# Optimization experiments

Hardware: AMD Instinct MI355X
Metric: run time of the kernel (lower is better)

## Reference

```python
import jax, jax.numpy as jnp
import numpy as np

N, IN_DIM, HID = 8192, 256, 512
NEG_INF = jnp.float32(-1e30)


def _linear_params(key, fan_in, fan_out):
    k1, k2 = jax.random.split(key)
    bound = 1.0 / np.sqrt(fan_in)
    W = jax.random.uniform(k1, (fan_in, fan_out), jnp.float32, -bound, bound)
    b = jax.random.uniform(k2, (fan_out,), jnp.float32, -bound, bound)
    return W, b


def setup_inputs() -> dict:
    key = jax.random.key(0)
    ks = jax.random.split(key, 10)
    x = jax.random.normal(ks[0], (N, IN_DIM), jnp.float32)
    adj = jax.random.randint(ks[1], (N, N), 0, 2) > 0
    adj = adj | jnp.eye(N, dtype=bool)  # self-loops: no all-masked rows
    Win, b_in = _linear_params(ks[2], IN_DIM, HID)
    Wq, bq = _linear_params(ks[3], HID, HID)
    Wk, bk = _linear_params(ks[4], HID, HID)
    Wv, bv = _linear_params(ks[5], HID, HID)
    Wo, bo = _linear_params(ks[6], HID, HID)
    Ws, bs = _linear_params(ks[7], HID, 1)
    Wf1, bf1 = _linear_params(ks[8], HID, HID)
    Wf2, bf2 = _linear_params(ks[9], HID, HID)
    g1 = jnp.ones((HID,), jnp.float32); be1 = jnp.zeros((HID,), jnp.float32)
    g2 = jnp.ones((HID,), jnp.float32); be2 = jnp.zeros((HID,), jnp.float32)
    return dict(x=x, adj=adj, Win=Win, b_in=b_in, Wq=Wq, bq=bq, Wk=Wk, bk=bk,
                Wv=Wv, bv=bv, Wo=Wo, bo=bo, Ws=Ws, bs=bs,
                g1=g1, be1=be1, g2=g2, be2=be2,
                Wf1=Wf1, bf1=bf1, Wf2=Wf2, bf2=bf2)


def _layernorm(x, g, b, eps=1e-5):
    mu = jnp.mean(x, axis=-1, keepdims=True)
    var = jnp.mean(jnp.square(x - mu), axis=-1, keepdims=True)
    return (x - mu) * jax.lax.rsqrt(var + eps) * g + b


def reference(x, adj, Win, b_in, Wq, bq, Wk, bk, Wv, bv, Wo, bo, Ws, bs,
              g1, be1, g2, be2, Wf1, bf1, Wf2, bf2):
    h = x @ Win + b_in                      # [N, HID]
    q = h @ Wq + bq
    k = h @ Wk + bk
    v = h @ Wv + bv
    scale = 1.0 / np.sqrt(HID).astype(np.float32)
    scores = (q @ k.T) * scale              # [N, N]
    scores = jnp.where(adj, scores, NEG_INF)
    attn = jax.nn.softmax(scores, axis=-1)  # dropout = identity (eval mode)
    h2 = attn @ v                           # [N, HID]
    h = _layernorm(h + (h2 @ Wo + bo), g1, be1)
    ff = jnp.maximum(h @ Wf1 + bf1, 0.0) @ Wf2 + bf2
    h = _layernorm(h + ff, g2, be2)
    logits = (h @ Ws + bs).squeeze(-1)      # [N]
    return logits
```

## Files before the change

kernel.cpp:

```cpp
#include <hip/hip_runtime.h>

typedef unsigned int u32;
typedef unsigned short u16;
typedef unsigned char u8;

typedef __bf16 bf16_t;
typedef bf16_t bf16x8 __attribute__((ext_vector_type(8)));
typedef float f32x4 __attribute__((ext_vector_type(4)));

#define NROW 8192
#define HID 512
#define DIN 256
#define LDQ 1536
#define NSPLIT 4
#define KVCH (NROW / NSPLIT)
#define KVB 64

__device__ __forceinline__ u16 f2b(float f) {
    u32 u = __float_as_uint(f);
    u32 r = (u + 0x7fffu + ((u >> 16) & 1u)) >> 16;
    return (u16)r;
}
__device__ __forceinline__ float b2f(u16 h) {
    return __uint_as_float(((u32)h) << 16);
}
__device__ __forceinline__ f32x4 zero4() {
    f32x4 z = {0.f, 0.f, 0.f, 0.f};
    return z;
}
__device__ __forceinline__ void gll16(const void* g, void* l) {
    __builtin_amdgcn_global_load_lds(
        (const __attribute__((address_space(1))) unsigned int*)g,
        (__attribute__((address_space(3))) unsigned int*)l, 16, 0, 0);
}

__global__ void sniff_adj(const u32* __restrict__ adj, int* __restrict__ mode) {
    __shared__ int f01[4], ff32[4], fbf[4];
    int t = threadIdx.x, lane = t & 63, wv = t >> 6;
    int all01 = 1, allf32 = 1, allbf = 1;
    for (int i = t; i < 1024; i += 256) {
        u32 w = adj[i];
        if (w > 1u) all01 = 0;
        if (w != 0u && w != 0x3f800000u) allf32 = 0;
    }
    const u16* h = (const u16*)adj;
    for (int i = t; i < 2048; i += 256) {
        u16 v = h[i];
        if (v != 0 && v != 0x3f80u) allbf = 0;
    }
    all01 = __all(all01);
    allf32 = __all(allf32);
    allbf = __all(allbf);
    if (lane == 0) { f01[wv] = all01; ff32[wv] = allf32; fbf[wv] = allbf; }
    __syncthreads();
    if (t == 0) {
        int a = f01[0] & f01[1] & f01[2] & f01[3];
        int b = ff32[0] & ff32[1] & ff32[2] & ff32[3];
        int c = fbf[0] & fbf[1] & fbf[2] & fbf[3];
        mode[0] = a ? 0 : (b ? 1 : (c ? 2 : 3));
    }
}

__global__ __launch_bounds__(256) void build_bits(const void* __restrict__ adj,
                                                  const int* __restrict__ mode,
                                                  u32* __restrict__ bits) {
    int row = blockIdx.x;
    int t = threadIdx.x;
    int lane = t & 63, wv = t >> 6;
    int md = *mode;
    for (int c0 = 0; c0 < NROW; c0 += 256) {
        int c = c0 + t;
        size_t idx = (size_t)row * NROW + c;
        bool nz;
        if (md == 0)      nz = ((const u32*)adj)[idx] != 0u;
        else if (md == 1) nz = ((const float*)adj)[idx] != 0.f;
        else if (md == 2) nz = ((const u16*)adj)[idx] != 0;
        else              nz = ((const u8*)adj)[idx] != 0;
        unsigned long long bm = __ballot(nz);
        if (lane == 0) {
            int w = row * 256 + (c0 >> 5) + wv * 2;
            bits[w] = (u32)bm;
            bits[w + 1] = (u32)(bm >> 32);
        }
    }
}

__global__ __launch_bounds__(256) void convert_f32_bf16(const float* __restrict__ in,
                                                        u16* __restrict__ out, int n) {
    int i = blockIdx.x * 256 + threadIdx.x;
    if (i < n) out[i] = f2b(in[i]);
}

__global__ __launch_bounds__(256) void transpose_wt(const float* __restrict__ W,
                                                    u16* __restrict__ out, int R, int C) {
    __shared__ u16 tile[64][65];
    int c0 = blockIdx.x * 64, r0 = blockIdx.y * 64;
    int t = threadIdx.x;
#pragma unroll
    for (int i = 0; i < 16; i++) {
        int idx = t + i * 256;
        int rr = idx >> 6, cc = idx & 63;
        tile[rr][cc] = f2b(W[(size_t)(r0 + rr) * C + c0 + cc]);
    }
    __syncthreads();
#pragma unroll
    for (int i = 0; i < 16; i++) {
        int idx = t + i * 256;
        int rr = idx >> 6, cc = idx & 63;
        out[(size_t)(c0 + rr) * R + r0 + cc] = tile[cc][rr];
    }
}

__global__ void concat_bias(const float* __restrict__ bq, const float* __restrict__ bk,
                            const float* __restrict__ bv, float* __restrict__ out) {
    int i = blockIdx.x * 256 + threadIdx.x;
    if (i >= 1536) return;
    out[i] = i < 512 ? bq[i] : (i < 1024 ? bk[i - 512] : bv[i - 1024]);
}

__global__ __launch_bounds__(256) void transpose_v_tiled(const u16* __restrict__ in, int ldv,
                                                         u16* __restrict__ out) {
    __shared__ u16 tl[64][72];
    int c0 = blockIdx.x * 64;
    int r0 = blockIdx.y * 64;
    int t = threadIdx.x;
#pragma unroll
    for (int i = 0; i < 2; i++) {
        int idx = t + i * 256;
        int rr = idx >> 3, ck = idx & 7;
        bf16x8 v = *(const bf16x8*)(in + (size_t)(r0 + rr) * ldv + c0 + ck * 8);
#pragma unroll
        for (int j = 0; j < 8; j++) tl[ck * 8 + j][rr] = ((u16*)&v)[j];
    }
    __syncthreads();
#pragma unroll
    for (int i = 0; i < 2; i++) {
        int idx = t + i * 256;
        int col = idx >> 3, ch = idx & 7;
        int kv = ch * 8;
        bf16x8 v;
#pragma unroll
        for (int j = 0; j < 8; j++) ((u16*)&v)[j] = tl[col][kv + j];
        *(bf16x8*)(out + (size_t)((r0 + kv) >> 5) * (HID * 32) +
                   (size_t)(c0 + col) * 32 + (kv & 31)) = v;
    }
}

__global__ __launch_bounds__(256, 3) void gemm_k(const u16* __restrict__ A, int lda,
                                                 const u16* __restrict__ Bt,
                                                 const float* __restrict__ bias,
                                                 const float* __restrict__ resid,
                                                 float* __restrict__ outF,
                                                 u16* __restrict__ outH, int ldo,
                                                 int relu, int K) {
    __shared__ u16 Ald[2][8192];
    __shared__ u16 Bld[2][4096];
    int t = threadIdx.x;
    int lane = t & 63, wave = t >> 6;
    int l15 = lane & 15, lg = lane >> 4;
    int row0 = blockIdx.y * 128, col0 = blockIdx.x * 64;

    auto stage = [&](int buf, int kk) {
#pragma unroll
        for (int p = 0; p < 4; p++) {
            int idx = p * 256 + t;
            int row = idx >> 3, c = idx & 7;
            gll16(A + (size_t)(row0 + row) * lda + kk + ((c ^ (row & 7)) * 8),
                  &Ald[buf][idx * 8]);
        }
#pragma unroll
        for (int p = 0; p < 2; p++) {
            int idx = p * 256 + t;
            int row = idx >> 3, c = idx & 7;
            gll16(Bt + (size_t)(col0 + row) * K + kk + ((c ^ (row & 7)) * 8),
                  &Bld[buf][idx * 8]);
        }
    };

    f32x4 acc[2][4];
#pragma unroll
    for (int i = 0; i < 2; i++)
#pragma unroll
        for (int j = 0; j < 4; j++) acc[i][j] = zero4();

    stage(0, 0);
    asm volatile("s_waitcnt vmcnt(0)" ::: "memory");
    __syncthreads();

    int nk = K >> 6;
    for (int kt = 0; kt < nk; kt++) {
        int buf = kt & 1;
        if (kt + 1 < nk) stage(buf ^ 1, (kt + 1) * 64);
#pragma unroll
        for (int ks = 0; ks < 2; ks++) {
            bf16x8 af[2], bfr[4];
#pragma unroll
            for (int i = 0; i < 2; i++) {
                int row = wave * 32 + i * 16 + l15;
                af[i] = *(const bf16x8*)&Ald[buf][row * 64 + (((ks * 4 + lg) ^ (row & 7)) * 8)];
            }
#pragma unroll
            for (int j = 0; j < 4; j++) {
                int row = j * 16 + l15;
                bfr[j] = *(const bf16x8*)&Bld[buf][row * 64 + (((ks * 4 + lg) ^ (row & 7)) * 8)];
            }
            __builtin_amdgcn_s_setprio(1);
#pragma unroll
            for (int i = 0; i < 2; i++)
#pragma unroll
                for (int j = 0; j < 4; j++)
                    acc[i][j] = __builtin_amdgcn_mfma_f32_16x16x32_bf16(af[i], bfr[j],
                                                                       acc[i][j], 0, 0, 0);
            __builtin_amdgcn_s_setprio(0);
        }
        asm volatile("s_waitcnt vmcnt(0)" ::: "memory");
        __syncthreads();
    }
#pragma unroll
    for (int j = 0; j < 4; j++) {
        int col = col0 + j * 16 + l15;
        float bv = bias[col];
#pragma unroll
        for (int i = 0; i < 2; i++) {
#pragma unroll
            for (int r = 0; r < 4; r++) {
                int row = row0 + wave * 32 + i * 16 + lg * 4 + r;
                float v = acc[i][j][r] + bv;
                if (relu) v = fmaxf(v, 0.f);
                size_t o = (size_t)row * ldo + col;
                if (resid) v += resid[o];
                if (outF) outF[o] = v;
                if (outH) outH[o] = f2b(v);
            }
        }
    }
}

__global__ __launch_bounds__(512, 2) void attn_kernel(const u16* __restrict__ QKV,
                                                      const u16* __restrict__ VTt,
                                                      const u32* __restrict__ bits,
                                                      u16* __restrict__ Opart,
                                                      float* __restrict__ Mpart,
                                                      float* __restrict__ Lpart) {
    extern __shared__ char smem[];
    u16* Klds = (u16*)smem;
    u16* Plds = (u16*)(smem + 131072);
    float* cscL = (float*)(smem + 147456);
    int* flagsL = (int*)(smem + 147968);
    int lane = threadIdx.x & 63, wave = threadIdx.x >> 6;
    int l15 = lane & 15, lg = lane >> 4;
    int s = blockIdx.x & 3;
    int qb = blockIdx.x >> 2;
    int qrow0 = qb * 128;
    int myrows = qrow0 + wave * 16;
    const u16* Kg = QKV + 512;

    bf16x8 qf[16];
    {
        const u16* qp = QKV + (size_t)(myrows + l15) * LDQ + lg * 8;
#pragma unroll
        for (int ks = 0; ks < 16; ks++) qf[ks] = *(const bf16x8*)(qp + ks * 32);
    }

    f32x4 acc[8][4];
#pragma unroll
    for (int i = 0; i < 8; i++)
#pragma unroll
        for (int j = 0; j < 4; j++) acc[i][j] = zero4();
    float m[4] = {-1e30f, -1e30f, -1e30f, -1e30f};
    float lsum[4] = {0.f, 0.f, 0.f, 0.f};
    const float scale = 0.04419417382415922f;
    int kvbeg = s * KVCH;

    auto STAGE = [&](int buf, int kv0) {
#pragma unroll
        for (int i = 0; i < 8; i++) {
            int seg = wave * 8 + i;
            int ks = seg >> 2, q = seg & 3;
            gll16(Kg + (size_t)(kv0 + q * 16 + l15) * LDQ + ks * 32 + lg * 8,
                  Klds + buf * 32768 + seg * 512 + lane * 8);
        }
    };

    STAGE(0, kvbeg);
    asm volatile("s_waitcnt vmcnt(0)" ::: "memory");
    __syncthreads();

    const int NT = KVCH / KVB;
    for (int t = 0; t < NT; ++t) {
        int kv0 = kvbeg + t * KVB;
        int buf = t & 1;
        const u16* kb = Klds + buf * 32768;

        f32x4 sf[4];
#pragma unroll
        for (int f = 0; f < 4; f++) sf[f] = zero4();
        __builtin_amdgcn_s_setprio(1);
#pragma unroll
        for (int ks = 0; ks < 16; ks++) {
#pragma unroll
            for (int q = 0; q < 4; q++) {
                bf16x8 b = *(const bf16x8*)(kb + (ks * 4 + q) * 512 + lane * 8);
                sf[q] = __builtin_amdgcn_mfma_f32_16x16x32_bf16(qf[ks], b, sf[q], 0, 0, 0);
            }
        }
        __builtin_amdgcn_s_setprio(0);

        u32 w0[4], w1[4];
#pragma unroll
        for (int r = 0; r < 4; r++) {
            const u32* wp = bits + (size_t)(myrows + lg * 4 + r) * 256 + (kv0 >> 5);
            w0[r] = wp[0];
            w1[r] = wp[1];
        }
        float pvv[4][4];
        float mx[4] = {-1e30f, -1e30f, -1e30f, -1e30f};
#pragma unroll
        for (int f = 0; f < 4; f++) {
            int c = f * 16 + l15;
#pragma unroll
            for (int r = 0; r < 4; r++) {
                u32 w = (c < 32) ? w0[r] : w1[r];
                bool bit = (w >> (c & 31)) & 1u;
                float sv = bit ? sf[f][r] * scale : -1e30f;
                pvv[f][r] = sv;
                mx[r] = fmaxf(mx[r], sv);
            }
        }
        bool need = false;
#pragma unroll
        for (int r = 0; r < 4; r++) need |= (mx[r] > m[r] + 8.0f);
        int wneed = __any(need ? 1 : 0);
        float cscv[4] = {1.f, 1.f, 1.f, 1.f};
        if (wneed) {
#pragma unroll
            for (int r = 0; r < 4; r++) {
#pragma unroll
                for (int off = 8; off; off >>= 1)
                    mx[r] = fmaxf(mx[r], __shfl_xor(mx[r], off, 64));
                float mn = fmaxf(m[r], mx[r]);
                cscv[r] = __expf(m[r] - mn);
                m[r] = mn;
                lsum[r] *= cscv[r];
            }
        }
        if (l15 == 0) *(f32x4*)&cscL[wave * 16 + lg * 4] = *(f32x4*)cscv;
        if (lane == 0) flagsL[wave] = wneed;

#pragma unroll
        for (int f = 0; f < 4; f++)
#pragma unroll
            for (int r = 0; r < 4; r++)
                pvv[f][r] = (pvv[f][r] < -1e29f) ? 0.f : __expf(pvv[f][r] - m[r]);
#pragma unroll
        for (int r = 0; r < 4; r++)
            lsum[r] += pvv[0][r] + pvv[1][r] + pvv[2][r] + pvv[3][r];

#pragma unroll
        for (int f = 0; f < 4; f++)
#pragma unroll
            for (int r = 0; r < 4; r++)
                Plds[(wave * 2 + (f >> 1)) * 512 + ((f & 1) * 2 + (l15 >> 3)) * 128 +
                     (lg * 4 + r) * 8 + (l15 & 7)] = f2b(pvv[f][r]);

        asm volatile("s_waitcnt lgkmcnt(0)" ::: "memory");
        __builtin_amdgcn_sched_barrier(0);
        __builtin_amdgcn_s_barrier();
        __builtin_amdgcn_sched_barrier(0);

        if (t + 1 < NT) STAGE(buf ^ 1, kv0 + KVB);

        int anyf = __any(flagsL[lane & 7] != 0);
        if (anyf) {
#pragma unroll
            for (int rf = 0; rf < 8; rf++) {
                f32x4 cs = *(const f32x4*)&cscL[rf * 16 + lg * 4];
#pragma unroll
                for (int cf = 0; cf < 4; cf++) {
                    f32x4 a = acc[rf][cf];
                    a[0] *= cs[0]; a[1] *= cs[1]; a[2] *= cs[2]; a[3] *= cs[3];
                    acc[rf][cf] = a;
                }
            }
        }

#pragma unroll
        for (int ks = 0; ks < 2; ks++) {
            const u16* vbase = VTt + (size_t)((kv0 >> 5) + ks) * (HID * 32) +
                               (size_t)wave * 64 * 32;
            bf16x8 vv[4];
#pragma unroll
            for (int cf = 0; cf < 4; cf++)
                vv[cf] = *(const bf16x8*)(vbase + (size_t)(cf * 16 + l15) * 32 + lg * 8);
            __builtin_amdgcn_s_setprio(1);
#pragma unroll
            for (int rf = 0; rf < 8; rf++) {
                bf16x8 pa = *(const bf16x8*)(Plds + (rf * 2 + ks) * 512 + lane * 8);
#pragma unroll
                for (int cf = 0; cf < 4; cf++)
                    acc[rf][cf] = __builtin_amdgcn_mfma_f32_16x16x32_bf16(pa, vv[cf],
                                                                         acc[rf][cf], 0, 0, 0);
            }
            __builtin_amdgcn_s_setprio(0);
        }

        asm volatile("s_waitcnt vmcnt(0) lgkmcnt(0)" ::: "memory");
        __builtin_amdgcn_sched_barrier(0);
        __builtin_amdgcn_s_barrier();
        __builtin_amdgcn_sched_barrier(0);
    }

#pragma unroll
    for (int r = 0; r < 4; r++) {
#pragma unroll
        for (int off = 8; off; off >>= 1)
            lsum[r] += __shfl_xor(lsum[r], off, 64);
    }
    if (l15 == 0) {
#pragma unroll
        for (int r = 0; r < 4; r++) {
            size_t o = (size_t)s * NROW + myrows + lg * 4 + r;
            Mpart[o] = m[r];
            Lpart[o] = lsum[r];
        }
    }
#pragma unroll
    for (int rf = 0; rf < 8; rf++)
#pragma unroll
        for (int cf = 0; cf < 4; cf++) {
            int col = wave * 64 + cf * 16 + l15;
#pragma unroll
            for (int j = 0; j < 4; j++) {
                size_t row = (size_t)s * NROW + qrow0 + rf * 16 + lg * 4 + j;
                Opart[row * HID + col] = f2b(acc[rf][cf][j]);
            }
        }
}

__global__ __launch_bounds__(256) void attn_combine(const u16* __restrict__ Opart,
                                                    const float* __restrict__ Mpart,
                                                    const float* __restrict__ Lpart,
                                                    u16* __restrict__ O16) {
    int idx = blockIdx.x * 256 + threadIdx.x;
    int row = idx >> 6;
    int c8 = (idx & 63) << 3;
    float ms[NSPLIT], M = -1e30f;
#pragma unroll
    for (int s = 0; s < NSPLIT; s++) {
        ms[s] = Mpart[(size_t)s * NROW + row];
        M = fmaxf(M, ms[s]);
    }
    float w[NSPLIT], L = 0.f;
#pragma unroll
    for (int s = 0; s < NSPLIT; s++) {
        w[s] = __expf(ms[s] - M);
        L += Lpart[(size_t)s * NROW + row] * w[s];
    }
    float inv = 1.f / L;
    float o[8];
#pragma unroll
    for (int j = 0; j < 8; j++) o[j] = 0.f;
#pragma unroll
    for (int s = 0; s < NSPLIT; s++) {
        bf16x8 p = *(const bf16x8*)(Opart + ((size_t)s * NROW + row) * HID + c8);
#pragma unroll
        for (int j = 0; j < 8; j++) o[j] += (float)p[j] * w[s];
    }
    bf16x8 res;
#pragma unroll
    for (int j = 0; j < 8; j++) {
        u16 b = f2b(o[j] * inv);
        res[j] = *(bf16_t*)&b;
    }
    *(bf16x8*)(O16 + (size_t)row * HID + c8) = res;
}

__global__ __launch_bounds__(256) void ln_single(const float* __restrict__ a,
                                                 const float* __restrict__ g,
                                                 const float* __restrict__ be,
                                                 float* __restrict__ outF,
                                                 u16* __restrict__ outH) {
    int row = blockIdx.x, t = threadIdx.x;
    const float* ar = a + (size_t)row * HID;
    float x0 = ar[t];
    float x1 = ar[t + 256];
    float s = x0 + x1, s2 = x0 * x0 + x1 * x1;
#pragma unroll
    for (int off = 32; off; off >>= 1) {
        s += __shfl_xor(s, off, 64);
        s2 += __shfl_xor(s2, off, 64);
    }
    __shared__ float ls[4], ls2[4];
    int wv = t >> 6, ln = t & 63;
    if (ln == 0) { ls[wv] = s; ls2[wv] = s2; }
    __syncthreads();
    float S = ls[0] + ls[1] + ls[2] + ls[3];
    float S2 = ls2[0] + ls2[1] + ls2[2] + ls2[3];
    float mu = S * (1.f / 512.f);
    float var = S2 * (1.f / 512.f) - mu * mu;
    float inv = rsqrtf(var + 1e-5f);
    float y0 = (x0 - mu) * inv * g[t] + be[t];
    float y1 = (x1 - mu) * inv * g[t + 256] + be[t + 256];
    size_t o = (size_t)row * HID + t;
    if (outF) { outF[o] = y0; outF[o + 256] = y1; }
    if (outH) { outH[o] = f2b(y0); outH[o + 256] = f2b(y1); }
}

__global__ __launch_bounds__(256) void logits_k(const u16* __restrict__ hfin,
                                                const float* __restrict__ Ws,
                                                const float* __restrict__ bs,
                                                float* __restrict__ out) {
    int row = blockIdx.x * 4 + (threadIdx.x >> 6);
    int lane = threadIdx.x & 63;
    const u16* hp = hfin + (size_t)row * HID + lane * 8;
    float sum = 0.f;
#pragma unroll
    for (int j = 0; j < 8; j++) sum += b2f(hp[j]) * Ws[lane * 8 + j];
#pragma unroll
    for (int off = 32; off; off >>= 1) sum += __shfl_xor(sum, off, 64);
    if (lane == 0) out[row] = sum + bs[0];
}

extern "C" void kernel_launch(void* const* d_in, const int* in_sizes, int n_in,
                              void* d_out, int out_size, void* d_ws, size_t ws_size,
                              hipStream_t stream) {
    const float* x   = (const float*)d_in[0];
    const void*  adj = d_in[1];
    const float* Win = (const float*)d_in[2];
    const float* b_in= (const float*)d_in[3];
    const float* Wq  = (const float*)d_in[4];
    const float* bq  = (const float*)d_in[5];
    const float* Wk  = (const float*)d_in[6];
    const float* bk  = (const float*)d_in[7];
    const float* Wv  = (const float*)d_in[8];
    const float* bv  = (const float*)d_in[9];
    const float* Wo  = (const float*)d_in[10];
    const float* bo  = (const float*)d_in[11];
    const float* Ws  = (const float*)d_in[12];
    const float* bs  = (const float*)d_in[13];
    const float* g1  = (const float*)d_in[14];
    const float* be1 = (const float*)d_in[15];
    const float* g2  = (const float*)d_in[16];
    const float* be2 = (const float*)d_in[17];
    const float* Wf1 = (const float*)d_in[18];
    const float* bf1 = (const float*)d_in[19];
    const float* Wf2 = (const float*)d_in[20];
    const float* bf2 = (const float*)d_in[21];

    char* ws = (char*)d_ws;
    const size_t MB = 1u << 20;
    const size_t OFF_PART = 0;
    const size_t OFF_X16  = 0;
    const size_t OFF_H16  = 4 * MB;
    const size_t OFF_HN32 = 12 * MB;
    const size_t OFF_HN16 = 28 * MB;
    const size_t OFF_FF1  = 4 * MB;
    const size_t OFF_HF32 = 36 * MB;
    const size_t OFF_QKV  = 52 * MB;
    const size_t OFF_OP32 = 52 * MB;
    const size_t OFF_FF2  = 52 * MB;
    const size_t OFF_VT   = 76 * MB;
    const size_t OFF_HFIN = 76 * MB;
    const size_t OFF_H2   = 84 * MB;
    const size_t OFF_BITS = 92 * MB;
    size_t off = 100 * MB;
    const size_t OFF_WINT = off;  off += 262144;
    const size_t OFF_QKVT = off;  off += 1572864;
    const size_t OFF_WOT  = off;  off += 524288;
    const size_t OFF_WF1T = off;  off += 524288;
    const size_t OFF_WF2T = off;  off += 524288;
    const size_t OFF_BQKV = off;  off += 8192;
    const size_t OFF_MODE = off;  off += 4096;
    const size_t OFF_MPART= off;  off += 131072;
    const size_t OFF_LPART= off;  off += 131072;

    u16* pX16   = (u16*)(ws + OFF_X16);
    u16* pH16   = (u16*)(ws + OFF_H16);
    float* pHN32= (float*)(ws + OFF_HN32);
    u16* pHN16  = (u16*)(ws + OFF_HN16);
    u16* pFF1   = (u16*)(ws + OFF_FF1);
    float* pHF32= (float*)(ws + OFF_HF32);
    u16* pQKV   = (u16*)(ws + OFF_QKV);
    float* pOP32= (float*)(ws + OFF_OP32);
    float* pFF2 = (float*)(ws + OFF_FF2);
    u16* pVT    = (u16*)(ws + OFF_VT);
    u16* pHFIN  = (u16*)(ws + OFF_HFIN);
    u16* pH2    = (u16*)(ws + OFF_H2);
    u32* pBits  = (u32*)(ws + OFF_BITS);
    u16* pPart  = (u16*)(ws + OFF_PART);
    u16* pWinT  = (u16*)(ws + OFF_WINT);
    u16* pQKVT  = (u16*)(ws + OFF_QKVT);
    u16* pWoT   = (u16*)(ws + OFF_WOT);
    u16* pWf1T  = (u16*)(ws + OFF_WF1T);
    u16* pWf2T  = (u16*)(ws + OFF_WF2T);
    float* pBqkv= (float*)(ws + OFF_BQKV);
    int* pMode  = (int*)(ws + OFF_MODE);
    float* pMp  = (float*)(ws + OFF_MPART);
    float* pLp  = (float*)(ws + OFF_LPART);

    sniff_adj<<<1, 256, 0, stream>>>((const u32*)adj, pMode);
    build_bits<<<NROW, 256, 0, stream>>>(adj, pMode, pBits);

    convert_f32_bf16<<<(NROW * DIN) / 256, 256, 0, stream>>>(x, pX16, NROW * DIN);
    transpose_wt<<<dim3(8, 4), 256, 0, stream>>>(Win, pWinT, DIN, HID);
    transpose_wt<<<dim3(8, 8), 256, 0, stream>>>(Wq, pQKVT, HID, HID);
    transpose_wt<<<dim3(8, 8), 256, 0, stream>>>(Wk, pQKVT + 512 * 512, HID, HID);
    transpose_wt<<<dim3(8, 8), 256, 0, stream>>>(Wv, pQKVT + 2 * 512 * 512, HID, HID);
    transpose_wt<<<dim3(8, 8), 256, 0, stream>>>(Wo, pWoT, HID, HID);
    transpose_wt<<<dim3(8, 8), 256, 0, stream>>>(Wf1, pWf1T, HID, HID);
    transpose_wt<<<dim3(8, 8), 256, 0, stream>>>(Wf2, pWf2T, HID, HID);
    concat_bias<<<6, 256, 0, stream>>>(bq, bk, bv, pBqkv);

    gemm_k<<<dim3(8, 64), 256, 0, stream>>>(pX16, DIN, pWinT, b_in, nullptr,
                                            pHF32, pH16, HID, 0, DIN);
    gemm_k<<<dim3(24, 64), 256, 0, stream>>>(pH16, HID, pQKVT, pBqkv, nullptr,
                                             nullptr, pQKV, LDQ, 0, HID);
    transpose_v_tiled<<<dim3(HID / 64, NROW / 64), 256, 0, stream>>>(pQKV + 1024, LDQ, pVT);
    attn_kernel<<<64 * NSPLIT, 512, 148032, stream>>>(pQKV, pVT, pBits, pPart, pMp, pLp);
    attn_combine<<<NROW * HID / (256 * 8), 256, 0, stream>>>(pPart, pMp, pLp, pH2);
    gemm_k<<<dim3(8, 64), 256, 0, stream>>>(pH2, HID, pWoT, bo, pHF32,
                                            pOP32, nullptr, HID, 0, HID);
    ln_single<<<NROW, 256, 0, stream>>>(pOP32, g1, be1, pHN32, pHN16);
    gemm_k<<<dim3(8, 64), 256, 0, stream>>>(pHN16, HID, pWf1T, bf1, nullptr,
                                            nullptr, pFF1, HID, 1, HID);
    gemm_k<<<dim3(8, 64), 256, 0, stream>>>(pFF1, HID, pWf2T, bf2, pHN32,
                                            pFF2, nullptr, HID, 0, HID);
    ln_single<<<NROW, 256, 0, stream>>>(pFF2, g2, be2, nullptr, pHFIN);
    logits_k<<<NROW / 4, 256, 0, stream>>>(pHFIN, Ws, bs, (float*)d_out);
}
```

Baseline: 502.1 us.

## Retile attention to 64-row, 4-wave blocks and fuse prep and final LN kernels

The attention kernel now runs 4-wave blocks on 64 query rows with 32-key tiles, so LDS use per block roughly halves and twice as many blocks launch. Each wave now owns 128 output columns instead of 64. Separately, the weight transposes, x conversion and bias concat are merged into one prep launch, and the second layernorm is fused with the logits dot product. Together these cut launch overhead and an intermediate bf16 buffer. The smaller tiles mean more loop iterations and barriers per key, and the V fragment loads are reused across fewer query rows.

```diff
diff --git a/kernel.cpp b/kernel.cpp
--- a/kernel.cpp
+++ b/kernel.cpp
@@ -14,7 +14,7 @@
 #define LDQ 1536
 #define NSPLIT 4
 #define KVCH (NROW / NSPLIT)
-#define KVB 64
+#define KVB 32
 
 __device__ __forceinline__ u16 f2b(float f) {
     u32 u = __float_as_uint(f);
@@ -34,9 +34,13 @@
         (__attribute__((address_space(3))) unsigned int*)l, 16, 0, 0);
 }
 
-__global__ void sniff_adj(const u32* __restrict__ adj, int* __restrict__ mode) {
+__global__ void sniff_and_bias(const u32* __restrict__ adj, int* __restrict__ mode,
+                               const float* __restrict__ bq, const float* __restrict__ bk,
+                               const float* __restrict__ bv, float* __restrict__ bqkv) {
     __shared__ int f01[4], ff32[4], fbf[4];
     int t = threadIdx.x, lane = t & 63, wv = t >> 6;
+    for (int i = t; i < 1536; i += 256)
+        bqkv[i] = i < 512 ? bq[i] : (i < 1024 ? bk[i - 512] : bv[i - 1024]);
     int all01 = 1, allf32 = 1, allbf = 1;
     for (int i = t; i < 1024; i += 256) {
         u32 w = adj[i];
@@ -85,37 +89,59 @@
     }
 }
 
-__global__ __launch_bounds__(256) void convert_f32_bf16(const float* __restrict__ in,
-                                                        u16* __restrict__ out, int n) {
-    int i = blockIdx.x * 256 + threadIdx.x;
-    if (i < n) out[i] = f2b(in[i]);
-}
-
-__global__ __launch_bounds__(256) void transpose_wt(const float* __restrict__ W,
-                                                    u16* __restrict__ out, int R, int C) {
+__global__ __launch_bounds__(256) void prep(const float* __restrict__ x,
+                                            const float* __restrict__ Win,
+                                            const float* __restrict__ Wq,
+                                            const float* __restrict__ Wk,
+                                            const float* __restrict__ Wv,
+                                            const float* __restrict__ Wo,
+                                            const float* __restrict__ Wf1,
+                                            const float* __restrict__ Wf2,
+                                            u16* __restrict__ pX16,
+                                            u16* __restrict__ pWinT,
+                                            u16* __restrict__ pQKVT,
+                                            u16* __restrict__ pWoT,
+                                            u16* __restrict__ pWf1T,
+                                            u16* __restrict__ pWf2T) {
+    int z = blockIdx.z;
+    int t = threadIdx.x;
+    if (z == 7) {
+        size_t base = ((size_t)blockIdx.y * 8 + blockIdx.x) * 32768;
+#pragma unroll 4
+        for (int k = 0; k < 128; k++) {
+            size_t i = base + k * 256 + t;
+            pX16[i] = f2b(x[i]);
+        }
+        return;
+    }
+    const float* src;
+    u16* dst;
+    int R = 512;
+    switch (z) {
+        case 0: src = Win; dst = pWinT; R = 256; break;
+        case 1: src = Wq;  dst = pQKVT; break;
+        case 2: src = Wk;  dst = pQKVT + 512 * 512; break;
+        case 3: src = Wv;  dst = pQKVT + 2 * 512 * 512; break;
+        case 4: src = Wo;  dst = pWoT; break;
+        case 5: src = Wf1; dst = pWf1T; break;
+        default: src = Wf2; dst = pWf2T; break;
+    }
+    int r0 = blockIdx.y * 64, c0 = blockIdx.x * 64;
+    if (r0 >= R) return;
     __shared__ u16 tile[64][65];
-    int c0 = blockIdx.x * 64, r0 = blockIdx.y * 64;
-    int t = threadIdx.x;
 #pragma unroll
     for (int i = 0; i < 16; i++) {
         int idx = t + i * 256;
         int rr = idx >> 6, cc = idx & 63;
-        tile[rr][cc] = f2b(W[(size_t)(r0 + rr) * C + c0 + cc]);
+        tile[rr][cc] = f2b(src[(size_t)(r0 + rr) * 512 + c0 + cc]);
     }
     __syncthreads();
 #pragma unroll
     for (int i = 0; i < 16; i++) {
         int idx = t + i * 256;
         int rr = idx >> 6, cc = idx & 63;
-        out[(size_t)(c0 + rr) * R + r0 + cc] = tile[cc][rr];
-    }
-}
-
-__global__ void concat_bias(const float* __restrict__ bq, const float* __restrict__ bk,
-                            const float* __restrict__ bv, float* __restrict__ out) {
-    int i = blockIdx.x * 256 + threadIdx.x;
-    if (i >= 1536) return;
-    out[i] = i < 512 ? bq[i] : (i < 1024 ? bk[i - 512] : bv[i - 1024]);
+        dst[(size_t)(c0 + rr) * R + r0 + cc] = tile[cc][rr];
+    }
 }
 
 __global__ __launch_bounds__(256) void transpose_v_tiled(const u16* __restrict__ in, int ldv,
@@ -236,7 +262,7 @@
     }
 }
 
-__global__ __launch_bounds__(512, 2) void attn_kernel(const u16* __restrict__ QKV,
+__global__ __launch_bounds__(256, 2) void attn_kernel(const u16* __restrict__ QKV,
                                                       const u16* __restrict__ VTt,
                                                       const u32* __restrict__ bits,
                                                       u16* __restrict__ Opart,
@@ -244,14 +270,14 @@
                                                       float* __restrict__ Lpart) {
     extern __shared__ char smem[];
     u16* Klds = (u16*)smem;
-    u16* Plds = (u16*)(smem + 131072);
-    float* cscL = (float*)(smem + 147456);
-    int* flagsL = (int*)(smem + 147968);
+    u16* Plds = (u16*)(smem + 65536);
+    float* cscL = (float*)(smem + 69632);
+    int* flagsL = (int*)(smem + 69888);
     int lane = threadIdx.x & 63, wave = threadIdx.x >> 6;
     int l15 = lane & 15, lg = lane >> 4;
-    int s = blockIdx.x & 3;
-    int qb = blockIdx.x >> 2;
-    int qrow0 = qb * 128;
+    int s = blockIdx.x >> 7;
+    int qb = blockIdx.x & 127;
+    int qrow0 = qb * 64;
     int myrows = qrow0 + wave * 16;
     const u16* Kg = QKV + 512;
 
@@ -262,11 +288,11 @@
         for (int ks = 0; ks < 16; ks++) qf[ks] = *(const bf16x8*)(qp + ks * 32);
     }
 
-    f32x4 acc[8][4];
-#pragma unroll
-    for (int i = 0; i < 8; i++)
-#pragma unroll
-        for (int j = 0; j < 4; j++) acc[i][j] = zero4();
+    f32x4 acc[4][8];
+#pragma unroll
+    for (int i = 0; i < 4; i++)
+#pragma unroll
+        for (int j = 0; j < 8; j++) acc[i][j] = zero4();
     float m[4] = {-1e30f, -1e30f, -1e30f, -1e30f};
     float lsum[4] = {0.f, 0.f, 0.f, 0.f};
     const float scale = 0.04419417382415922f;
@@ -276,9 +302,9 @@
 #pragma unroll
         for (int i = 0; i < 8; i++) {
             int seg = wave * 8 + i;
-            int ks = seg >> 2, q = seg & 3;
+            int ks = seg >> 1, q = seg & 1;
             gll16(Kg + (size_t)(kv0 + q * 16 + l15) * LDQ + ks * 32 + lg * 8,
-                  Klds + buf * 32768 + seg * 512 + lane * 8);
+                  Klds + buf * 16384 + seg * 512 + lane * 8);
         }
     };
 
@@ -290,38 +316,32 @@
     for (int t = 0; t < NT; ++t) {
         int kv0 = kvbeg + t * KVB;
         int buf = t & 1;
-        const u16* kb = Klds + buf * 32768;
-
-        f32x4 sf[4];
-#pragma unroll
-        for (int f = 0; f < 4; f++) sf[f] = zero4();
+        const u16* kb = Klds + buf * 16384;
+
+        f32x4 sf[2];
+        sf[0] = zero4(); sf[1] = zero4();
         __builtin_amdgcn_s_setprio(1);
 #pragma unroll
         for (int ks = 0; ks < 16; ks++) {
-#pragma unroll
-            for (int q = 0; q < 4; q++) {
-                bf16x8 b = *(const bf16x8*)(kb + (ks * 4 + q) * 512 + lane * 8);
-                sf[q] = __builtin_amdgcn_mfma_f32_16x16x32_bf16(qf[ks], b, sf[q], 0, 0, 0);
-            }
+            bf16x8 b0 = *(const bf16x8*)(kb + (ks * 2) * 512 + lane * 8);
+            bf16x8 b1 = *(const bf16x8*)(kb + (ks * 2 + 1) * 512 + lane * 8);
+            sf[0] = __builtin_amdgcn_mfma_f32_16x16x32_bf16(qf[ks], b0, sf[0], 0, 0, 0);
+            sf[1] = __builtin_amdgcn_mfma_f32_16x16x32_bf16(qf[ks], b1, sf[1], 0, 0, 0);
         }
         __builtin_amdgcn_s_setprio(0);
 
-        u32 w0[4], w1[4];
-#pragma unroll
-        for (int r = 0; r < 4; r++) {
-            const u32* wp = bits + (size_t)(myrows + lg * 4 + r) * 256 + (kv0 >> 5);
-            w0[r] = wp[0];
-            w1[r] = wp[1];
-        }
-        float pvv[4][4];
+        u32 w0[4];
+#pragma unroll
+        for (int r = 0; r < 4; r++)
+            w0[r] = bits[(size_t)(myrows + lg * 4 + r) * 256 + (kv0 >> 5)];
+        float pvv[2][4];
         float mx[4] = {-1e30f, -1e30f, -1e30f, -1e30f};
 #pragma unroll
-        for (int f = 0; f < 4; f++) {
+        for (int f = 0; f < 2; f++) {
             int c = f * 16 + l15;
 #pragma unroll
             for (int r = 0; r < 4; r++) {
-                u32 w = (c < 32) ? w0[r] : w1[r];
-                bool bit = (w >> (c & 31)) & 1u;
+                bool bit = (w0[r] >> c) & 1u;
                 float sv = bit ? sf[f][r] * scale : -1e30f;
                 pvv[f][r] = sv;
                 mx[r] = fmaxf(mx[r], sv);
@@ -348,20 +368,20 @@
         if (lane == 0) flagsL[wave] = wneed;
 
 #pragma unroll
-        for (int f = 0; f < 4; f++)
+        for (int f = 0; f < 2; f++)
 #pragma unroll
             for (int r = 0; r < 4; r++)
                 pvv[f][r] = (pvv[f][r] < -1e29f) ? 0.f : __expf(pvv[f][r] - m[r]);
 #pragma unroll
         for (int r = 0; r < 4; r++)
-            lsum[r] += pvv[0][r] + pvv[1][r] + pvv[2][r] + pvv[3][r];
-
-#pragma unroll
-        for (int f = 0; f < 4; f++)
+            lsum[r] += pvv[0][r] + pvv[1][r];
+
+#pragma unroll
+        for (int f = 0; f < 2; f++)
 #pragma unroll
             for (int r = 0; r < 4; r++)
-                Plds[(wave * 2 + (f >> 1)) * 512 + ((f & 1) * 2 + (l15 >> 3)) * 128 +
-                     (lg * 4 + r) * 8 + (l15 & 7)] = f2b(pvv[f][r]);
+                Plds[wave * 512 + (f * 2 + (l15 >> 3)) * 128 + (lg * 4 + r) * 8 + (l15 & 7)] =
+                    f2b(pvv[f][r]);
 
         asm volatile("s_waitcnt lgkmcnt(0)" ::: "memory");
         __builtin_amdgcn_sched_barrier(0);
@@ -370,13 +390,13 @@
 
         if (t + 1 < NT) STAGE(buf ^ 1, kv0 + KVB);
 
-        int anyf = __any(flagsL[lane & 7] != 0);
+        int anyf = __any(flagsL[lane & 3] != 0);
         if (anyf) {
 #pragma unroll
-            for (int rf = 0; rf < 8; rf++) {
+            for (int rf = 0; rf < 4; rf++) {
                 f32x4 cs = *(const f32x4*)&cscL[rf * 16 + lg * 4];
 #pragma unroll
-                for (int cf = 0; cf < 4; cf++) {
+                for (int cf = 0; cf < 8; cf++) {
                     f32x4 a = acc[rf][cf];
                     a[0] *= cs[0]; a[1] *= cs[1]; a[2] *= cs[2]; a[3] *= cs[3];
                     acc[rf][cf] = a;
@@ -385,21 +405,21 @@
         }
 
 #pragma unroll
-        for (int ks = 0; ks < 2; ks++) {
-            const u16* vbase = VTt + (size_t)((kv0 >> 5) + ks) * (HID * 32) +
-                               (size_t)wave * 64 * 32;
+        for (int g2 = 0; g2 < 2; g2++) {
+            const u16* vb = VTt + (size_t)(kv0 >> 5) * (HID * 32) +
+                            (size_t)(wave * 128 + g2 * 64) * 32;
             bf16x8 vv[4];
 #pragma unroll
-            for (int cf = 0; cf < 4; cf++)
-                vv[cf] = *(const bf16x8*)(vbase + (size_t)(cf * 16 + l15) * 32 + lg * 8);
+            for (int c4 = 0; c4 < 4; c4++)
+                vv[c4] = *(const bf16x8*)(vb + (size_t)(c4 * 16 + l15) * 32 + lg * 8);
             __builtin_amdgcn_s_setprio(1);
 #pragma unroll
-            for (int rf = 0; rf < 8; rf++) {
-                bf16x8 pa = *(const bf16x8*)(Plds + (rf * 2 + ks) * 512 + lane * 8);
-#pragma unroll
-                for (int cf = 0; cf < 4; cf++)
-                    acc[rf][cf] = __builtin_amdgcn_mfma_f32_16x16x32_bf16(pa, vv[cf],
-                                                                         acc[rf][cf], 0, 0, 0);
+            for (int rf = 0; rf < 4; rf++) {
+                bf16x8 pa = *(const bf16x8*)(Plds + rf * 512 + lane * 8);
+#pragma unroll
+                for (int c4 = 0; c4 < 4; c4++)
+                    acc[rf][g2 * 4 + c4] = __builtin_amdgcn_mfma_f32_16x16x32_bf16(
+                        pa, vv[c4], acc[rf][g2 * 4 + c4], 0, 0, 0);
             }
             __builtin_amdgcn_s_setprio(0);
         }
@@ -425,10 +445,10 @@
         }
     }
 #pragma unroll
-    for (int rf = 0; rf < 8; rf++)
-#pragma unroll
-        for (int cf = 0; cf < 4; cf++) {
-            int col = wave * 64 + cf * 16 + l15;
+    for (int rf = 0; rf < 4; rf++)
+#pragma unroll
+        for (int cf = 0; cf < 8; cf++) {
+            int col = wave * 128 + cf * 16 + l15;
 #pragma unroll
             for (int j = 0; j < 4; j++) {
                 size_t row = (size_t)s * NROW + qrow0 + rf * 16 + lg * 4 + j;
@@ -502,23 +522,43 @@
     float y0 = (x0 - mu) * inv * g[t] + be[t];
     float y1 = (x1 - mu) * inv * g[t + 256] + be[t + 256];
     size_t o = (size_t)row * HID + t;
-    if (outF) { outF[o] = y0; outF[o + 256] = y1; }
-    if (outH) { outH[o] = f2b(y0); outH[o + 256] = f2b(y1); }
-}
-
-__global__ __launch_bounds__(256) void logits_k(const u16* __restrict__ hfin,
-                                                const float* __restrict__ Ws,
-                                                const float* __restrict__ bs,
-                                                float* __restrict__ out) {
-    int row = blockIdx.x * 4 + (threadIdx.x >> 6);
-    int lane = threadIdx.x & 63;
-    const u16* hp = hfin + (size_t)row * HID + lane * 8;
-    float sum = 0.f;
-#pragma unroll
-    for (int j = 0; j < 8; j++) sum += b2f(hp[j]) * Ws[lane * 8 + j];
-#pragma unroll
-    for (int off = 32; off; off >>= 1) sum += __shfl_xor(sum, off, 64);
-    if (lane == 0) out[row] = sum + bs[0];
+    outF[o] = y0; outF[o + 256] = y1;
+    outH[o] = f2b(y0); outH[o + 256] = f2b(y1);
+}
+
+__global__ __launch_bounds__(256) void ln_logits(const float* __restrict__ a,
+                                                 const float* __restrict__ g,
+                                                 const float* __restrict__ be,
+                                                 const float* __restrict__ Ws,
+                                                 const float* __restrict__ bs,
+                                                 float* __restrict__ out) {
+    int row = blockIdx.x, t = threadIdx.x;
+    const float* ar = a + (size_t)row * HID;
+    float x0 = ar[t];
+    float x1 = ar[t + 256];
+    float s = x0 + x1, s2 = x0 * x0 + x1 * x1;
+#pragma unroll
+    for (int off = 32; off; off >>= 1) {
+        s += __shfl_xor(s, off, 64);
+        s2 += __shfl_xor(s2, off, 64);
+    }
+    __shared__ float ls[4], ls2[4], lp[4];
+    int wv = t >> 6, ln = t & 63;
+    if (ln == 0) { ls[wv] = s; ls2[wv] = s2; }
+    __syncthreads();
+    float S = ls[0] + ls[1] + ls[2] + ls[3];
+    float S2 = ls2[0] + ls2[1] + ls2[2] + ls2[3];
+    float mu = S * (1.f / 512.f);
+    float var = S2 * (1.f / 512.f) - mu * mu;
+    float inv = rsqrtf(var + 1e-5f);
+    float y0 = (x0 - mu) * inv * g[t] + be[t];
+    float y1 = (x1 - mu) * inv * g[t + 256] + be[t + 256];
+    float p = y0 * Ws[t] + y1 * Ws[t + 256];
+#pragma unroll
+    for (int off = 32; off; off >>= 1) p += __shfl_xor(p, off, 64);
+    if (ln == 0) lp[wv] = p;
+    __syncthreads();
+    if (t == 0) out[row] = lp[0] + lp[1] + lp[2] + lp[3] + bs[0];
 }
 
 extern "C" void kernel_launch(void* const* d_in, const int* in_sizes, int n_in,
@@ -560,7 +600,6 @@
     const size_t OFF_OP32 = 52 * MB;
     const size_t OFF_FF2  = 52 * MB;
     const size_t OFF_VT   = 76 * MB;
-    const size_t OFF_HFIN = 76 * MB;
     const size_t OFF_H2   = 84 * MB;
     const size_t OFF_BITS = 92 * MB;
     size_t off = 100 * MB;
@@ -584,7 +623,6 @@
     float* pOP32= (float*)(ws + OFF_OP32);
     float* pFF2 = (float*)(ws + OFF_FF2);
     u16* pVT    = (u16*)(ws + OFF_VT);
-    u16* pHFIN  = (u16*)(ws + OFF_HFIN);
     u16* pH2    = (u16*)(ws + OFF_H2);
     u32* pBits  = (u32*)(ws + OFF_BITS);
     u16* pPart  = (u16*)(ws + OFF_PART);
@@ -598,25 +636,18 @@
     float* pMp  = (float*)(ws + OFF_MPART);
     float* pLp  = (float*)(ws + OFF_LPART);
 
-    sniff_adj<<<1, 256, 0, stream>>>((const u32*)adj, pMode);
+    sniff_and_bias<<<1, 256, 0, stream>>>((const u32*)adj, pMode, bq, bk, bv, pBqkv);
     build_bits<<<NROW, 256, 0, stream>>>(adj, pMode, pBits);
 
-    convert_f32_bf16<<<(NROW * DIN) / 256, 256, 0, stream>>>(x, pX16, NROW * DIN);
-    transpose_wt<<<dim3(8, 4), 256, 0, stream>>>(Win, pWinT, DIN, HID);
-    transpose_wt<<<dim3(8, 8), 256, 0, stream>>>(Wq, pQKVT, HID, HID);
-    transpose_wt<<<dim3(8, 8), 256, 0, stream>>>(Wk, pQKVT + 512 * 512, HID, HID);
-    transpose_wt<<<dim3(8, 8), 256, 0, stream>>>(Wv, pQKVT + 2 * 512 * 512, HID, HID);
-    transpose_wt<<<dim3(8, 8), 256, 0, stream>>>(Wo, pWoT, HID, HID);
-    transpose_wt<<<dim3(8, 8), 256, 0, stream>>>(Wf1, pWf1T, HID, HID);
-    transpose_wt<<<dim3(8, 8), 256, 0, stream>>>(Wf2, pWf2T, HID, HID);
-    concat_bias<<<6, 256, 0, stream>>>(bq, bk, bv, pBqkv);
+    prep<<<dim3(8, 8, 8), 256, 0, stream>>>(x, Win, Wq, Wk, Wv, Wo, Wf1, Wf2,
+                                            pX16, pWinT, pQKVT, pWoT, pWf1T, pWf2T);
 
     gemm_k<<<dim3(8, 64), 256, 0, stream>>>(pX16, DIN, pWinT, b_in, nullptr,
                                             pHF32, pH16, HID, 0, DIN);
     gemm_k<<<dim3(24, 64), 256, 0, stream>>>(pH16, HID, pQKVT, pBqkv, nullptr,
                                              nullptr, pQKV, LDQ, 0, HID);
     transpose_v_tiled<<<dim3(HID / 64, NROW / 64), 256, 0, stream>>>(pQKV + 1024, LDQ, pVT);
-    attn_kernel<<<64 * NSPLIT, 512, 148032, stream>>>(pQKV, pVT, pBits, pPart, pMp, pLp);
+    attn_kernel<<<128 * NSPLIT, 256, 69920, stream>>>(pQKV, pVT, pBits, pPart, pMp, pLp);
     attn_combine<<<NROW * HID / (256 * 8), 256, 0, stream>>>(pPart, pMp, pLp, pH2);
     gemm_k<<<dim3(8, 64), 256, 0, stream>>>(pH2, HID, pWoT, bo, pHF32,
                                             pOP32, nullptr, HID, 0, HID);
@@ -625,6 +656,5 @@
                                             nullptr, pFF1, HID, 1, HID);
     gemm_k<<<dim3(8, 64), 256, 0, stream>>>(pFF1, HID, pWf2T, bf2, pHN32,
                                             pFF2, nullptr, HID, 0, HID);
-    ln_single<<<NROW, 256, 0, stream>>>(pFF2, g2, be2, nullptr, pHFIN);
-    logits_k<<<NROW / 4, 256, 0, stream>>>(pHFIN, Ws, bs, (float*)d_out);
-}
+    ln_logits<<<NROW, 256, 0, stream>>>(pFF2, g2, be2, Ws, bs, (float*)d_out);
+}
```

New measurement: 551.2 us. 9.8% more time.
